# Kernel optimization log

Measured on AMD Instinct MI355X. Metric: run time of the kernel, lower is better.

Reference implementation:

```python
import jax, jax.numpy as jnp
import numpy as np

N_NODES = 100000
N_EDGES = 50000
NNZ = 800000
D_IN = 128
D_OUT = 128


def setup_inputs() -> dict:
    key = jax.random.key(0)
    k1, k2, k3, k4, k5 = jax.random.split(key, 5)
    x_0 = jax.random.normal(k1, (N_NODES, D_IN), dtype=jnp.float32)
    W = jax.random.normal(k2, (D_OUT, D_IN), dtype=jnp.float32) / np.sqrt(D_IN)
    b = jax.random.normal(k3, (D_OUT,), dtype=jnp.float32) * 0.01
    node_ids = jax.random.randint(k4, (NNZ,), 0, N_NODES, dtype=jnp.int32)
    edge_ids = jax.random.randint(k5, (NNZ,), 0, N_EDGES, dtype=jnp.int32)
    return {"x_0": x_0, "W": W, "b": b, "node_ids": node_ids, "edge_ids": edge_ids}


def reference(x_0, W, b, node_ids, edge_ids):
    # Linear transform (no batchnorm: use_bn=False)
    x = x_0 @ W.T + b  # [n_nodes, out_channels]

    # Step 1: hyperedge aggregation (e_aggr='sum'):  m_{0->1} = B_1^T x, reduce=sum
    m01 = jax.ops.segment_sum(x[node_ids], edge_ids, num_segments=N_EDGES)  # [n_edges, d]

    # Step 2: node aggregation (v_aggr='mean'):  m_{1->0} = B_1 m_{0->1}, reduce=mean
    s = jax.ops.segment_sum(m01[edge_ids], node_ids, num_segments=N_NODES)  # [n_nodes, d]
    cnt = jax.ops.segment_sum(jnp.ones((NNZ,), dtype=x.dtype), node_ids, num_segments=N_NODES)
    m10 = s / jnp.maximum(cnt, 1.0)[:, None]

    # Step 3: SAGE update (residual add)
    return x + m10
```

## Files before the change

### kernel.cpp

```cpp
#include <hip/hip_runtime.h>
#include <hip/hip_bf16.h>

#define NN 100000
#define NE 50000
#define NZ 800000
#define D  128
#define NSEG (NE + NN)
#define FILL_P 8
#define FILL_B 3125

typedef __bf16 bf16x8 __attribute__((ext_vector_type(8)));
typedef float f32x4 __attribute__((ext_vector_type(4)));

static __device__ __forceinline__ unsigned short f2bf(float f) {
  union { float f; unsigned u; } v; v.f = f;
  unsigned r = (v.u + 0x7FFFu + ((v.u >> 16) & 1u)) >> 16;
  return (unsigned short)r;
}
static __device__ __forceinline__ float bf2f(unsigned short h) {
  union { unsigned u; float f; } v; v.u = ((unsigned)h) << 16;
  return v.f;
}

__global__ __launch_bounds__(256) void unisage_gemm_mfma(const float* __restrict__ x0,
                                                         const float* __restrict__ W,
                                                         const float* __restrict__ bias,
                                                         unsigned short* __restrict__ xb) {
  __shared__ __bf16 Wl[128][136];
  const int t = threadIdx.x;
#pragma unroll
  for (int i = 0; i < 16; ++i) {
    int idx = i * 1024 + t * 4;
    int dout = idx >> 7;
    int k = idx & 127;
    float4 wv = *(const float4*)(W + idx);
    Wl[dout][k + 0] = (__bf16)wv.x;
    Wl[dout][k + 1] = (__bf16)wv.y;
    Wl[dout][k + 2] = (__bf16)wv.z;
    Wl[dout][k + 3] = (__bf16)wv.w;
  }
  __syncthreads();

  const int wave = t >> 6;
  const int lane = t & 63;
  const int lr = lane & 15;
  const int lg = lane >> 4;
  const int rowbase = blockIdx.x * 128 + wave * 32;

  f32x4 acc[2][8] = {};

#pragma unroll
  for (int ks = 0; ks < 4; ++ks) {
    const int k0 = ks * 32 + lg * 8;
    bf16x8 b[8];
#pragma unroll
    for (int cf = 0; cf < 8; ++cf)
      b[cf] = *(const bf16x8*)&Wl[cf * 16 + lr][k0];
#pragma unroll
    for (int rf = 0; rf < 2; ++rf) {
      int row = rowbase + rf * 16 + lr;
      row = row < NN ? row : NN - 1;
      const float* src = x0 + (size_t)row * D + k0;
      float4 f0 = *(const float4*)(src);
      float4 f1 = *(const float4*)(src + 4);
      bf16x8 a;
      a[0] = (__bf16)f0.x; a[1] = (__bf16)f0.y;
      a[2] = (__bf16)f0.z; a[3] = (__bf16)f0.w;
      a[4] = (__bf16)f1.x; a[5] = (__bf16)f1.y;
      a[6] = (__bf16)f1.z; a[7] = (__bf16)f1.w;
#pragma unroll
      for (int cf = 0; cf < 8; ++cf)
        acc[rf][cf] = __builtin_amdgcn_mfma_f32_16x16x32_bf16(a, b[cf], acc[rf][cf], 0, 0, 0);
    }
  }

#pragma unroll
  for (int cf = 0; cf < 8; ++cf) {
    float bv = bias[cf * 16 + lr];
#pragma unroll
    for (int rf = 0; rf < 2; ++rf) {
#pragma unroll
      for (int r = 0; r < 4; ++r) {
        int row = rowbase + rf * 16 + lg * 4 + r;
        if (row < NN)
          xb[(size_t)row * D + cf * 16 + lr] = f2bf(acc[rf][cf][r] + bv);
      }
    }
  }
}

__global__ void unisage_hist_rank(const int* __restrict__ nid, const int* __restrict__ eid,
                                  int* __restrict__ cnt, unsigned int* __restrict__ rank) {
  int i = blockIdx.x * 256 + threadIdx.x;
  if (i >= NZ) return;
  int e = eid[i], v = nid[i];
  unsigned re = (unsigned)atomicAdd(&cnt[e], 1);
  unsigned rn = (unsigned)atomicAdd(&cnt[NE + v], 1);
  rank[i] = (re & 0xffffu) | (rn << 16);
}

__global__ void unisage_scan_k1(const int* __restrict__ in, int* __restrict__ bsum, int n) {
  __shared__ int sh[256];
  int t = threadIdx.x;
  int base = blockIdx.x * 1024 + t * 4;
  int s = 0;
#pragma unroll
  for (int j = 0; j < 4; ++j)
    if (base + j < n) s += in[base + j];
  sh[t] = s;
  __syncthreads();
  for (int o = 128; o > 0; o >>= 1) {
    if (t < o) sh[t] += sh[t + o];
    __syncthreads();
  }
  if (t == 0) bsum[blockIdx.x] = sh[0];
}

__global__ void unisage_scan_k2(const int* __restrict__ bsum, int* __restrict__ bsumx, int nb) {
  __shared__ int sh[256];
  int t = threadIdx.x;
  int v = (t < nb) ? bsum[t] : 0;
  sh[t] = v;
  __syncthreads();
  for (int o = 1; o < 256; o <<= 1) {
    int add = (t >= o) ? sh[t - o] : 0;
    __syncthreads();
    sh[t] += add;
    __syncthreads();
  }
  if (t < nb) bsumx[t] = sh[t] - v;
}

__global__ void unisage_scan_k3(const int* __restrict__ in, const int* __restrict__ bsumx,
                                int* __restrict__ out, int n) {
  __shared__ int sh[256];
  int t = threadIdx.x;
  int base = blockIdx.x * 1024 + t * 4;
  int v[4];
#pragma unroll
  for (int j = 0; j < 4; ++j) v[j] = (base + j < n) ? in[base + j] : 0;
  int tsum = v[0] + v[1] + v[2] + v[3];
  sh[t] = tsum;
  __syncthreads();
  for (int o = 1; o < 256; o <<= 1) {
    int add = (t >= o) ? sh[t - o] : 0;
    __syncthreads();
    sh[t] += add;
    __syncthreads();
  }
  int run = sh[t] - tsum + bsumx[blockIdx.x];
#pragma unroll
  for (int j = 0; j < 4; ++j) {
    if (base + j < n) out[base + j] = run;
    run += v[j];
  }
}

__global__ void unisage_fill(const int* __restrict__ nid, const int* __restrict__ eid,
                             const unsigned int* __restrict__ rank,
                             const int* __restrict__ off,
                             int* __restrict__ csr_e, int* __restrict__ csr_n) {
  const int R = (NSEG + FILL_P - 1) / FILL_P;
  int pass = blockIdx.x / FILL_B;
  int i = (blockIdx.x % FILL_B) * 256 + threadIdx.x;
  if (i >= NZ) return;
  int lo = pass * R, hi = lo + R;
  int e = eid[i], v = nid[i];
  unsigned r = rank[i];
  if (e >= lo && e < hi) csr_e[off[e] + (int)(r & 0xffffu)] = v;
  int s = NE + v;
  if (s >= lo && s < hi) csr_n[off[s] + (int)(r >> 16) - NZ] = e;
}

__global__ void unisage_edge_agg(const unsigned short* __restrict__ xb,
                                 const int* __restrict__ csr_e,
                                 const int* __restrict__ off, const int* __restrict__ cnt,
                                 unsigned short* __restrict__ m01b) {
  int w = (blockIdx.x * 256 + threadIdx.x) >> 6;
  int lane = threadIdx.x & 63;
  if (w >= NE) return;
  int beg = off[w];
  int end = beg + cnt[w];
  float ax = 0.f, ay = 0.f;
  for (int base = beg; base < end; base += 64) {
    int m = min(64, end - base);
    int idx = (lane < m) ? csr_e[base + lane] : 0;
    int j = 0;
    for (; j + 1 < m; j += 2) {
      int n0 = __shfl(idx, j, 64);
      int n1 = __shfl(idx, j + 1, 64);
      ushort2 a = *(const ushort2*)(xb + (size_t)n0 * D + lane * 2);
      ushort2 b = *(const ushort2*)(xb + (size_t)n1 * D + lane * 2);
      ax += bf2f(a.x) + bf2f(b.x);
      ay += bf2f(a.y) + bf2f(b.y);
    }
    if (j < m) {
      int n0 = __shfl(idx, j, 64);
      ushort2 a = *(const ushort2*)(xb + (size_t)n0 * D + lane * 2);
      ax += bf2f(a.x);
      ay += bf2f(a.y);
    }
  }
  ushort2 o; o.x = f2bf(ax); o.y = f2bf(ay);
  *(ushort2*)(m01b + (size_t)w * D + lane * 2) = o;
}

__global__ void unisage_node_agg(const unsigned short* __restrict__ xb,
                                 const unsigned short* __restrict__ m01b,
                                 const int* __restrict__ csr_n,
                                 const int* __restrict__ off, const int* __restrict__ cnt,
                                 float* __restrict__ out) {
  int w = (blockIdx.x * 256 + threadIdx.x) >> 6;
  int lane = threadIdx.x & 63;
  if (w >= NN) return;
  int deg = cnt[NE + w];
  int beg = off[NE + w] - NZ;
  int end = beg + deg;
  float ax = 0.f, ay = 0.f;
  for (int base = beg; base < end; base += 64) {
    int m = min(64, end - base);
    int idx = (lane < m) ? csr_n[base + lane] : 0;
    int j = 0;
    for (; j + 1 < m; j += 2) {
      int e0 = __shfl(idx, j, 64);
      int e1 = __shfl(idx, j + 1, 64);
      ushort2 a = *(const ushort2*)(m01b + (size_t)e0 * D + lane * 2);
      ushort2 b = *(const ushort2*)(m01b + (size_t)e1 * D + lane * 2);
      ax += bf2f(a.x) + bf2f(b.x);
      ay += bf2f(a.y) + bf2f(b.y);
    }
    if (j < m) {
      int e0 = __shfl(idx, j, 64);
      ushort2 a = *(const ushort2*)(m01b + (size_t)e0 * D + lane * 2);
      ax += bf2f(a.x);
      ay += bf2f(a.y);
    }
  }
  float inv = 1.0f / fmaxf((float)deg, 1.0f);
  ushort2 xr = *(const ushort2*)(xb + (size_t)w * D + lane * 2);
  float2 o;
  o.x = bf2f(xr.x) + ax * inv;
  o.y = bf2f(xr.y) + ay * inv;
  *(float2*)(out + (size_t)w * D + lane * 2) = o;
}

extern "C" void kernel_launch(void* const* d_in, const int* in_sizes, int n_in,
                              void* d_out, int out_size, void* d_ws, size_t ws_size,
                              hipStream_t stream) {
  const float* x0   = (const float*)d_in[0];
  const float* W    = (const float*)d_in[1];
  const float* bias = (const float*)d_in[2];
  const int* nid    = (const int*)d_in[3];
  const int* eid    = (const int*)d_in[4];
  float* out = (float*)d_out;

  unsigned short* xb   = (unsigned short*)d_ws;
  unsigned short* m01b = xb + (size_t)NN * D;
  int* cnt   = (int*)(m01b + (size_t)NE * D);
  int* off   = cnt + 150016;
  unsigned int* rank = (unsigned int*)(off + 150016);
  int* csr_e = (int*)(rank + NZ);
  int* csr_n = csr_e + NZ;
  int* bsum  = csr_n + NZ;
  int* bsumx = bsum + 256;

  hipMemsetAsync(cnt, 0, NSEG * sizeof(int), stream);

  unisage_gemm_mfma<<<(NN + 127) / 128, 256, 0, stream>>>(x0, W, bias, xb);

  unisage_hist_rank<<<NZ / 256, 256, 0, stream>>>(nid, eid, cnt, rank);

  const int nb = (NSEG + 1023) / 1024;
  unisage_scan_k1<<<nb, 256, 0, stream>>>(cnt, bsum, NSEG);
  unisage_scan_k2<<<1, 256, 0, stream>>>(bsum, bsumx, nb);
  unisage_scan_k3<<<nb, 256, 0, stream>>>(cnt, bsumx, off, NSEG);

  unisage_fill<<<FILL_P * FILL_B, 256, 0, stream>>>(nid, eid, rank, off, csr_e, csr_n);

  unisage_edge_agg<<<(NE * 64) / 256, 256, 0, stream>>>(xb, csr_e, off, cnt, m01b);
  unisage_node_agg<<<(NN * 64) / 256, 256, 0, stream>>>(xb, m01b, csr_n, off, cnt, out);
}
```

Before: 233.1 us.

## Vectorize hist/fill index loads, batch atomics, unroll gather loops by four

The histogram kernel now handles 8 entries per thread with int4 loads and batched atomics, and writes ranks as uint4. The fill kernel handles 4 entries per thread with vector loads, and its pass count drops from 8 to 4. Both aggregation kernels unroll the gather loop from 2 to 4 rows to keep more loads in flight. The aim is fewer instructions and more memory-level parallelism. In exchange, fewer threads and fewer fill passes may give worse scatter locality.

```diff
diff --git a/kernel.cpp b/kernel.cpp
--- a/kernel.cpp
+++ b/kernel.cpp
@@ -6,8 +6,8 @@
 #define NZ 800000
 #define D  128
 #define NSEG (NE + NN)
-#define FILL_P 8
-#define FILL_B 3125
+#define FILL_P 4
+#define FILL_B 782
 
 typedef __bf16 bf16x8 __attribute__((ext_vector_type(8)));
 typedef float f32x4 __attribute__((ext_vector_type(4)));
@@ -91,12 +91,30 @@
 
 __global__ void unisage_hist_rank(const int* __restrict__ nid, const int* __restrict__ eid,
                                   int* __restrict__ cnt, unsigned int* __restrict__ rank) {
-  int i = blockIdx.x * 256 + threadIdx.x;
-  if (i >= NZ) return;
-  int e = eid[i], v = nid[i];
-  unsigned re = (unsigned)atomicAdd(&cnt[e], 1);
-  unsigned rn = (unsigned)atomicAdd(&cnt[NE + v], 1);
-  rank[i] = (re & 0xffffu) | (rn << 16);
+  int base = (blockIdx.x * 256 + threadIdx.x) * 8;
+  if (base >= NZ) return;
+  int4 ea = *(const int4*)(eid + base);
+  int4 eb = *(const int4*)(eid + base + 4);
+  int4 na = *(const int4*)(nid + base);
+  int4 nb = *(const int4*)(nid + base + 4);
+  int e[8] = {ea.x, ea.y, ea.z, ea.w, eb.x, eb.y, eb.z, eb.w};
+  int v[8] = {na.x, na.y, na.z, na.w, nb.x, nb.y, nb.z, nb.w};
+  unsigned re[8], rn[8];
+#pragma unroll
+  for (int j = 0; j < 8; ++j) re[j] = (unsigned)atomicAdd(&cnt[e[j]], 1);
+#pragma unroll
+  for (int j = 0; j < 8; ++j) rn[j] = (unsigned)atomicAdd(&cnt[NE + v[j]], 1);
+  uint4 r0, r1;
+  r0.x = (re[0] & 0xffffu) | (rn[0] << 16);
+  r0.y = (re[1] & 0xffffu) | (rn[1] << 16);
+  r0.z = (re[2] & 0xffffu) | (rn[2] << 16);
+  r0.w = (re[3] & 0xffffu) | (rn[3] << 16);
+  r1.x = (re[4] & 0xffffu) | (rn[4] << 16);
+  r1.y = (re[5] & 0xffffu) | (rn[5] << 16);
+  r1.z = (re[6] & 0xffffu) | (rn[6] << 16);
+  r1.w = (re[7] & 0xffffu) | (rn[7] << 16);
+  *(uint4*)(rank + base) = r0;
+  *(uint4*)(rank + base + 4) = r1;
 }
 
 __global__ void unisage_scan_k1(const int* __restrict__ in, int* __restrict__ bsum, int n) {
@@ -162,14 +180,21 @@
                              int* __restrict__ csr_e, int* __restrict__ csr_n) {
   const int R = (NSEG + FILL_P - 1) / FILL_P;
   int pass = blockIdx.x / FILL_B;
-  int i = (blockIdx.x % FILL_B) * 256 + threadIdx.x;
-  if (i >= NZ) return;
+  int base = ((blockIdx.x % FILL_B) * 256 + threadIdx.x) * 4;
+  if (base >= NZ) return;
   int lo = pass * R, hi = lo + R;
-  int e = eid[i], v = nid[i];
-  unsigned r = rank[i];
-  if (e >= lo && e < hi) csr_e[off[e] + (int)(r & 0xffffu)] = v;
-  int s = NE + v;
-  if (s >= lo && s < hi) csr_n[off[s] + (int)(r >> 16) - NZ] = e;
+  int4 e4 = *(const int4*)(eid + base);
+  int4 n4 = *(const int4*)(nid + base);
+  uint4 r4 = *(const uint4*)(rank + base);
+  int e[4] = {e4.x, e4.y, e4.z, e4.w};
+  int v[4] = {n4.x, n4.y, n4.z, n4.w};
+  unsigned r[4] = {r4.x, r4.y, r4.z, r4.w};
+#pragma unroll
+  for (int j = 0; j < 4; ++j) {
+    if (e[j] >= lo && e[j] < hi) csr_e[off[e[j]] + (int)(r[j] & 0xffffu)] = v[j];
+    int s = NE + v[j];
+    if (s >= lo && s < hi) csr_n[off[s] + (int)(r[j] >> 16) - NZ] = e[j];
+  }
 }
 
 __global__ void unisage_edge_agg(const unsigned short* __restrict__ xb,
@@ -186,15 +211,19 @@
     int m = min(64, end - base);
     int idx = (lane < m) ? csr_e[base + lane] : 0;
     int j = 0;
-    for (; j + 1 < m; j += 2) {
+    for (; j + 3 < m; j += 4) {
       int n0 = __shfl(idx, j, 64);
       int n1 = __shfl(idx, j + 1, 64);
+      int n2 = __shfl(idx, j + 2, 64);
+      int n3 = __shfl(idx, j + 3, 64);
       ushort2 a = *(const ushort2*)(xb + (size_t)n0 * D + lane * 2);
       ushort2 b = *(const ushort2*)(xb + (size_t)n1 * D + lane * 2);
-      ax += bf2f(a.x) + bf2f(b.x);
-      ay += bf2f(a.y) + bf2f(b.y);
-    }
-    if (j < m) {
+      ushort2 c = *(const ushort2*)(xb + (size_t)n2 * D + lane * 2);
+      ushort2 d = *(const ushort2*)(xb + (size_t)n3 * D + lane * 2);
+      ax += (bf2f(a.x) + bf2f(b.x)) + (bf2f(c.x) + bf2f(d.x));
+      ay += (bf2f(a.y) + bf2f(b.y)) + (bf2f(c.y) + bf2f(d.y));
+    }
+    for (; j < m; ++j) {
       int n0 = __shfl(idx, j, 64);
       ushort2 a = *(const ushort2*)(xb + (size_t)n0 * D + lane * 2);
       ax += bf2f(a.x);
@@ -221,15 +250,19 @@
     int m = min(64, end - base);
     int idx = (lane < m) ? csr_n[base + lane] : 0;
     int j = 0;
-    for (; j + 1 < m; j += 2) {
+    for (; j + 3 < m; j += 4) {
       int e0 = __shfl(idx, j, 64);
       int e1 = __shfl(idx, j + 1, 64);
+      int e2 = __shfl(idx, j + 2, 64);
+      int e3 = __shfl(idx, j + 3, 64);
       ushort2 a = *(const ushort2*)(m01b + (size_t)e0 * D + lane * 2);
       ushort2 b = *(const ushort2*)(m01b + (size_t)e1 * D + lane * 2);
-      ax += bf2f(a.x) + bf2f(b.x);
-      ay += bf2f(a.y) + bf2f(b.y);
-    }
-    if (j < m) {
+      ushort2 c = *(const ushort2*)(m01b + (size_t)e2 * D + lane * 2);
+      ushort2 d = *(const ushort2*)(m01b + (size_t)e3 * D + lane * 2);
+      ax += (bf2f(a.x) + bf2f(b.x)) + (bf2f(c.x) + bf2f(d.x));
+      ay += (bf2f(a.y) + bf2f(b.y)) + (bf2f(c.y) + bf2f(d.y));
+    }
+    for (; j < m; ++j) {
       int e0 = __shfl(idx, j, 64);
       ushort2 a = *(const ushort2*)(m01b + (size_t)e0 * D + lane * 2);
       ax += bf2f(a.x);
@@ -268,7 +301,7 @@
 
   unisage_gemm_mfma<<<(NN + 127) / 128, 256, 0, stream>>>(x0, W, bias, xb);
 
-  unisage_hist_rank<<<NZ / 256, 256, 0, stream>>>(nid, eid, cnt, rank);
+  unisage_hist_rank<<<(NZ / 8 + 255) / 256, 256, 0, stream>>>(nid, eid, cnt, rank);
 
   const int nb = (NSEG + 1023) / 1024;
   unisage_scan_k1<<<nb, 256, 0, stream>>>(cnt, bsum, NSEG);
```

Measured after the change: 223.2 us. -4.2%, faster.
